# Kernel optimization log

Hardware: AMD Instinct MI355X
Metric: run time of the kernel (lower is better)

Reference implementation:

```python
import jax, jax.numpy as jnp
import numpy as np

N = 100000          # nodes
E = 1600000         # edges (before self loops)
IN, H, C, OUT = 128, 4, 32, 40
EPS = 1e-5          # BatchNorm eps
NEG_SLOPE = 0.2     # GATConv leaky_relu slope
BN_SCALE = 1.0 / np.sqrt(1.0 + EPS)  # eval BN with running mean 0, var 1


def gat_conv(x, W, att_src, att_dst, bias, src, dst, concat=True):
    """PyG GATConv (add_self_loops already applied to src/dst)."""
    heads, out_ch = att_src.shape
    n = x.shape[0]
    h = (x @ W).reshape(n, heads, out_ch)                 # [N,H,C]
    a_src = jnp.einsum('nhc,hc->nh', h, att_src)          # [N,H]
    a_dst = jnp.einsum('nhc,hc->nh', h, att_dst)          # [N,H]
    e = jax.nn.leaky_relu(a_src[src] + a_dst[dst], NEG_SLOPE)  # [E,H]
    # segment softmax over destination neighborhoods
    m = jax.ops.segment_max(e, dst, num_segments=n)
    e = jnp.exp(e - m[dst])
    s = jax.ops.segment_sum(e, dst, num_segments=n)
    alpha = e / (s[dst] + 1e-16)                          # [E,H]
    msg = h[src] * alpha[:, :, None]                      # [E,H,C]
    out = jax.ops.segment_sum(msg, dst, num_segments=n)   # [N,H,C]
    out = out.reshape(n, heads * out_ch) if concat else out.mean(axis=1)
    return out + bias


def setup_inputs():
    key = jax.random.key(0)
    ks = jax.random.split(key, 20)
    d = {}
    d['x'] = jax.random.normal(ks[0], (N, IN), dtype=jnp.float32)
    d['edge_index'] = jax.random.randint(ks[1], (2, E), 0, N, dtype=jnp.int32)
    sc = lambda fan: 1.0 / np.sqrt(fan)
    # layer 0: IN -> H*C
    d['W0'] = jax.random.normal(ks[2], (IN, H * C), dtype=jnp.float32) * sc(IN)
    d['as0'] = jax.random.normal(ks[3], (H, C), dtype=jnp.float32) * sc(C)
    d['ad0'] = jax.random.normal(ks[4], (H, C), dtype=jnp.float32) * sc(C)
    d['b0'] = jnp.zeros((H * C,), jnp.float32)
    d['g0'] = jnp.ones((H * C,), jnp.float32)
    d['be0'] = jnp.zeros((H * C,), jnp.float32)
    # layer 1: H*C -> H*C
    d['W1'] = jax.random.normal(ks[5], (H * C, H * C), dtype=jnp.float32) * sc(H * C)
    d['as1'] = jax.random.normal(ks[6], (H, C), dtype=jnp.float32) * sc(C)
    d['ad1'] = jax.random.normal(ks[7], (H, C), dtype=jnp.float32) * sc(C)
    d['b1'] = jnp.zeros((H * C,), jnp.float32)
    d['g1'] = jnp.ones((H * C,), jnp.float32)
    d['be1'] = jnp.zeros((H * C,), jnp.float32)
    # layer 2: H*C -> OUT, heads=1
    d['W2'] = jax.random.normal(ks[8], (H * C, OUT), dtype=jnp.float32) * sc(H * C)
    d['as2'] = jax.random.normal(ks[9], (1, OUT), dtype=jnp.float32) * sc(OUT)
    d['ad2'] = jax.random.normal(ks[10], (1, OUT), dtype=jnp.float32) * sc(OUT)
    d['b2'] = jnp.zeros((OUT,), jnp.float32)
    d['blast'] = jnp.zeros((OUT,), jnp.float32)
    return d


def reference(x, edge_index, W0, as0, ad0, b0, g0, be0,
              W1, as1, ad1, b1, g1, be1, W2, as2, ad2, b2, blast):
    loop = jnp.arange(N, dtype=edge_index.dtype)
    src = jnp.concatenate([edge_index[0], loop])
    dst = jnp.concatenate([edge_index[1], loop])
    h = gat_conv(x, W0, as0, ad0, b0, src, dst)
    h = jax.nn.relu(g0 * (h * BN_SCALE) + be0)   # eval BatchNorm + ReLU
    h = gat_conv(h, W1, as1, ad1, b1, src, dst)
    h = jax.nn.relu(g1 * (h * BN_SCALE) + be1)
    h = gat_conv(h, W2, as2, ad2, b2, src, dst)  # heads=1
    h = h + blast                                # ElementWiseLinear bias
    return jax.nn.log_softmax(h, axis=-1)
```

## Files before the change

### kernel.cpp

```cpp
#include <hip/hip_runtime.h>
#include <math.h>


static constexpr float BN_SCALE_F = 0.9999950000374996f;
static constexpr float NEG_SLOPE_F = 0.2f;

__global__ void k_deg(const int* __restrict__ ei, int E, int N, int* __restrict__ deg) {
    int i = blockIdx.x * 256 + threadIdx.x;
    int M = E + N;
    if (i >= M) return;
    int d = (i < E) ? ei[(size_t)E + i] : (i - E);
    atomicAdd(&deg[d], 1);
}

__global__ void k_scan1(const int* __restrict__ deg, int N, int* __restrict__ off,
                        int* __restrict__ bsum) {
    __shared__ int sh[2048];
    __shared__ int ts[256];
    int t = threadIdx.x;
    int base = blockIdx.x * 2048;
    for (int i = t; i < 2048; i += 256) sh[i] = (base + i < N) ? deg[base + i] : 0;
    __syncthreads();
    int loc[8];
    int tot = 0;
#pragma unroll
    for (int j = 0; j < 8; j++) { loc[j] = sh[t * 8 + j]; tot += loc[j]; }
    ts[t] = tot;
    __syncthreads();
    for (int d = 1; d < 256; d <<= 1) {
        int u = (t >= d) ? ts[t - d] : 0;
        __syncthreads();
        ts[t] += u;
        __syncthreads();
    }
    int run = (t > 0) ? ts[t - 1] : 0;
#pragma unroll
    for (int j = 0; j < 8; j++) {
        int idx = base + t * 8 + j;
        if (idx < N) off[idx] = run;
        run += loc[j];
    }
    if (t == 255) bsum[blockIdx.x] = ts[255];
}

__global__ void k_scan2(int* __restrict__ bsum, int nb) {
    __shared__ int ts[256];
    int t = threadIdx.x;
    int v = (t < nb) ? bsum[t] : 0;
    ts[t] = v;
    __syncthreads();
    for (int d = 1; d < 256; d <<= 1) {
        int u = (t >= d) ? ts[t - d] : 0;
        __syncthreads();
        ts[t] += u;
        __syncthreads();
    }
    if (t < nb) bsum[t] = ts[t] - v;
}

__global__ void k_scan3(int* __restrict__ off, const int* __restrict__ bsum, int N, int M) {
    int i = blockIdx.x * 256 + threadIdx.x;
    if (i < N) off[i] += bsum[i >> 11];
    else if (i == N) off[N] = M;
}

__global__ void k_scatter(const int* __restrict__ ei, int E, int N,
                          const int* __restrict__ off, int* __restrict__ cnt,
                          int* __restrict__ ssrc) {
    int i = blockIdx.x * 256 + threadIdx.x;
    int M = E + N;
    if (i >= M) return;
    int s, d;
    if (i < E) { s = ei[i]; d = ei[(size_t)E + i]; }
    else       { s = d = i - E; }
    int pos = off[d] + atomicAdd(&cnt[d], 1);
    ssrc[pos] = s;
}

template <int NC>
__global__ __launch_bounds__(512) void k_gemm(const float* __restrict__ A,
                                              const float* __restrict__ W, int N, int CC,
                                              int OST, float* __restrict__ out) {
    __shared__ float xs[128 * 128];
    __shared__ float ws[128 * NC];
    int tid = threadIdx.x;
    int row0 = blockIdx.x * 128;
    const float4* A4 = (const float4*)A;
#pragma unroll
    for (int i = 0; i < 8; i++) {
        int idx = tid + i * 512;
        int r = idx >> 5, c4 = idx & 31;
        int gr = row0 + r;
        float4 v = make_float4(0.f, 0.f, 0.f, 0.f);
        if (gr < N) v = A4[(size_t)gr * 32 + c4];
        int g = (r >> 3) & 3;
        *(float4*)&xs[r * 128 + ((c4 ^ g) << 2)] = v;
    }
    constexpr int WIT = (128 * NC) / (512 * 4);
#pragma unroll
    for (int i = 0; i < WIT; i++) {
        int idx = tid + i * 512;
        int k = idx / (NC / 4);
        int c = (idx % (NC / 4)) * 4;
        float4 v;
        if (c + 3 < CC) {
            v = *(const float4*)&W[(size_t)k * CC + c];
        } else {
            float tmp[4];
#pragma unroll
            for (int j = 0; j < 4; j++) tmp[j] = (c + j < CC) ? W[(size_t)k * CC + c + j] : 0.f;
            v = make_float4(tmp[0], tmp[1], tmp[2], tmp[3]);
        }
        *(float4*)&ws[k * NC + c] = v;
    }
    __syncthreads();

    int ty = tid >> 4;
    int tx = tid & 15;
    constexpr int NH = NC / 64;
    float4 acc[4][NH];
#pragma unroll
    for (int r = 0; r < 4; r++)
#pragma unroll
        for (int h = 0; h < NH; h++) acc[r][h] = make_float4(0.f, 0.f, 0.f, 0.f);

#pragma unroll 2
    for (int k4 = 0; k4 < 32; k4++) {
        float4 xv[4];
#pragma unroll
        for (int r = 0; r < 4; r++) {
            int row = ty * 4 + r;
            int g = (row >> 3) & 3;
            xv[r] = *(const float4*)&xs[row * 128 + (((k4 ^ g) & 31) << 2)];
        }
        float4 wv[4][NH];
#pragma unroll
        for (int j = 0; j < 4; j++)
#pragma unroll
            for (int h = 0; h < NH; h++)
                wv[j][h] = *(const float4*)&ws[(k4 * 4 + j) * NC + tx * 4 + 64 * h];
#pragma unroll
        for (int r = 0; r < 4; r++) {
            const float* xf = (const float*)&xv[r];
#pragma unroll
            for (int j = 0; j < 4; j++) {
                float xsv = xf[j];
#pragma unroll
                for (int h = 0; h < NH; h++) {
                    acc[r][h].x += xsv * wv[j][h].x;
                    acc[r][h].y += xsv * wv[j][h].y;
                    acc[r][h].z += xsv * wv[j][h].z;
                    acc[r][h].w += xsv * wv[j][h].w;
                }
            }
        }
    }
#pragma unroll
    for (int r = 0; r < 4; r++) {
        int gr = row0 + ty * 4 + r;
        if (gr >= N) continue;
#pragma unroll
        for (int h = 0; h < NH; h++) {
            int c = tx * 4 + 64 * h;
            if (c < CC) *(float4*)&out[(size_t)gr * OST + c] = acc[r][h];
        }
    }
}

__global__ void k_att(const float* __restrict__ h, const float* __restrict__ att_s,
                      const float* __restrict__ att_d, int N, float* __restrict__ asrc,
                      float* __restrict__ adst) {
    int wid = (blockIdx.x * 256 + threadIdx.x) >> 6;
    int lane = threadIdx.x & 63;
    if (wid >= N) return;
    float2 hv = *(const float2*)&h[(size_t)wid * 128 + lane * 2];
    float2 as_ = *(const float2*)&att_s[lane * 2];
    float2 ad_ = *(const float2*)&att_d[lane * 2];
    float ps = hv.x * as_.x + hv.y * as_.y;
    float pd = hv.x * ad_.x + hv.y * ad_.y;
    for (int d = 1; d < 16; d <<= 1) {
        ps += __shfl_xor(ps, d);
        pd += __shfl_xor(pd, d);
    }
    if ((lane & 15) == 0) {
        int hd = lane >> 4;
        asrc[(size_t)wid * 4 + hd] = ps;
        adst[(size_t)wid * 4 + hd] = pd;
    }
}

__global__ void k_att2(const float* __restrict__ h2, const float* __restrict__ as2,
                       const float* __restrict__ ad2, int N, float* __restrict__ asrc,
                       float* __restrict__ adst) {
    int wid = (blockIdx.x * 256 + threadIdx.x) >> 6;
    int lane = threadIdx.x & 63;
    if (wid >= N) return;
    float ps = 0.f, pd = 0.f;
    if (lane < 40) {
        float v = h2[(size_t)wid * 40 + lane];
        ps = v * as2[lane];
        pd = v * ad2[lane];
    }
    for (int d = 1; d < 64; d <<= 1) {
        ps += __shfl_xor(ps, d);
        pd += __shfl_xor(pd, d);
    }
    if (lane == 0) { asrc[wid] = ps; adst[wid] = pd; }
}

__global__ void k_agg(const float* __restrict__ h, const float* __restrict__ asrc,
                      const float* __restrict__ adst, const int* __restrict__ ssrc,
                      const int* __restrict__ off, const float* __restrict__ bias,
                      const float* __restrict__ gamma, const float* __restrict__ beta,
                      float* __restrict__ out, int N) {
    int wid = (blockIdx.x * 256 + threadIdx.x) >> 6;
    int lane = threadIdx.x & 63;
    if (wid >= N) return;
    int beg = off[wid], end = off[wid + 1];
    int hd = lane >> 4;
    float adst_h = adst[(size_t)wid * 4 + hd];
    float m = -INFINITY, ssum = 0.f, accx = 0.f, accy = 0.f;
    for (int j = beg; j < end; ++j) {
        int s = ssrc[j];
        float e = asrc[(size_t)s * 4 + hd] + adst_h;
        e = (e > 0.f) ? e : e * NEG_SLOPE_F;
        float mnew = fmaxf(m, e);
        float sc = __expf(m - mnew);
        float p = __expf(e - mnew);
        float2 hv = *(const float2*)&h[(size_t)s * 128 + lane * 2];
        ssum = ssum * sc + p;
        accx = accx * sc + p * hv.x;
        accy = accy * sc + p * hv.y;
        m = mnew;
    }
    float inv = 1.0f / (ssum + 1e-16f);
    int ch = lane * 2;
    float v0 = accx * inv + bias[ch];
    float v1 = accy * inv + bias[ch + 1];
    v0 = gamma[ch] * (v0 * BN_SCALE_F) + beta[ch];
    v1 = gamma[ch + 1] * (v1 * BN_SCALE_F) + beta[ch + 1];
    v0 = fmaxf(v0, 0.f);
    v1 = fmaxf(v1, 0.f);
    *(float2*)&out[(size_t)wid * 128 + ch] = make_float2(v0, v1);
}

__global__ void k_agg2(const float* __restrict__ h2, const float* __restrict__ asrc,
                       const float* __restrict__ adst, const int* __restrict__ ssrc,
                       const int* __restrict__ off, const float* __restrict__ b2,
                       const float* __restrict__ blast, float* __restrict__ out, int N) {
    int wid = (blockIdx.x * 256 + threadIdx.x) >> 6;
    int lane = threadIdx.x & 63;
    if (wid >= N) return;
    int beg = off[wid], end = off[wid + 1];
    float adn = adst[wid];
    int ch = lane;
    float m = -INFINITY, ssum = 0.f, acc = 0.f;
    for (int j = beg; j < end; ++j) {
        int s = ssrc[j];
        float e = asrc[s] + adn;
        e = (e > 0.f) ? e : e * NEG_SLOPE_F;
        float mnew = fmaxf(m, e);
        float sc = __expf(m - mnew);
        float p = __expf(e - mnew);
        float hv = (ch < 40) ? h2[(size_t)s * 40 + ch] : 0.f;
        ssum = ssum * sc + p;
        acc = acc * sc + p * hv;
        m = mnew;
    }
    float o = 0.f;
    if (ch < 40) o = acc / (ssum + 1e-16f) + b2[ch] + blast[ch];
    float lm = (ch < 40) ? o : -INFINITY;
    for (int d = 1; d < 64; d <<= 1) lm = fmaxf(lm, __shfl_xor(lm, d));
    float ex = (ch < 40) ? __expf(o - lm) : 0.f;
    float es = ex;
    for (int d = 1; d < 64; d <<= 1) es += __shfl_xor(es, d);
    if (ch < 40) out[(size_t)wid * 40 + ch] = o - lm - __logf(es);
}

extern "C" void kernel_launch(void* const* d_in, const int* in_sizes, int n_in, void* d_out,
                              int out_size, void* d_ws, size_t ws_size, hipStream_t stream) {
    const float* x   = (const float*)d_in[0];
    const int*   ei  = (const int*)d_in[1];
    const float* W0  = (const float*)d_in[2];
    const float* as0 = (const float*)d_in[3];
    const float* ad0 = (const float*)d_in[4];
    const float* b0  = (const float*)d_in[5];
    const float* g0  = (const float*)d_in[6];
    const float* be0 = (const float*)d_in[7];
    const float* W1  = (const float*)d_in[8];
    const float* as1 = (const float*)d_in[9];
    const float* ad1 = (const float*)d_in[10];
    const float* b1  = (const float*)d_in[11];
    const float* g1  = (const float*)d_in[12];
    const float* be1 = (const float*)d_in[13];
    const float* W2  = (const float*)d_in[14];
    const float* as2 = (const float*)d_in[15];
    const float* ad2 = (const float*)d_in[16];
    const float* b2  = (const float*)d_in[17];
    const float* bl  = (const float*)d_in[18];
    float* out = (float*)d_out;

    int N = in_sizes[0] / 128;
    int E = in_sizes[1] / 2;
    int M = E + N;

    char* p = (char*)d_ws;
    auto carve = [&](size_t bytes) -> char* {
        char* q = p;
        p += (bytes + 255) & ~(size_t)255;
        return q;
    };
    float* bufA = (float*)carve((size_t)N * 128 * 4);
    float* bufB = (float*)carve((size_t)N * 128 * 4);
    float* asrc = (float*)carve((size_t)N * 4 * 4);
    float* adst = (float*)carve((size_t)N * 4 * 4);
    int* deg  = (int*)carve((size_t)N * 4);
    int* off  = (int*)carve((size_t)(N + 1) * 4);
    int* bsum = (int*)carve(256 * 4);
    int* cnt  = (int*)carve((size_t)N * 4);
    int* ssrc = (int*)carve((size_t)M * 4);

    hipMemsetAsync(deg, 0, (size_t)N * 4, stream);
    hipMemsetAsync(cnt, 0, (size_t)N * 4, stream);
    k_deg<<<(M + 255) / 256, 256, 0, stream>>>(ei, E, N, deg);
    int NB = (N + 2047) / 2048;
    k_scan1<<<NB, 256, 0, stream>>>(deg, N, off, bsum);
    k_scan2<<<1, 256, 0, stream>>>(bsum, NB);
    k_scan3<<<(N + 256) / 256, 256, 0, stream>>>(off, bsum, N, M);
    k_scatter<<<(M + 255) / 256, 256, 0, stream>>>(ei, E, N, off, cnt, ssrc);

    int gblocks = (N + 127) / 128;
    int nodeblocks = (N + 3) / 4;

    k_gemm<128><<<gblocks, 512, 0, stream>>>(x, W0, N, 128, 128, bufA);
    k_att<<<nodeblocks, 256, 0, stream>>>(bufA, as0, ad0, N, asrc, adst);
    k_agg<<<nodeblocks, 256, 0, stream>>>(bufA, asrc, adst, ssrc, off, b0, g0, be0, bufB, N);
    k_gemm<128><<<gblocks, 512, 0, stream>>>(bufB, W1, N, 128, 128, bufA);
    k_att<<<nodeblocks, 256, 0, stream>>>(bufA, as1, ad1, N, asrc, adst);
    k_agg<<<nodeblocks, 256, 0, stream>>>(bufA, asrc, adst, ssrc, off, b1, g1, be1, bufB, N);
    k_gemm<64><<<gblocks, 512, 0, stream>>>(bufB, W2, N, 40, 40, bufA);
    k_att2<<<nodeblocks, 256, 0, stream>>>(bufA, as2, ad2, N, asrc, adst);
    k_agg2<<<nodeblocks, 256, 0, stream>>>(bufA, asrc, adst, ssrc, off, b2, bl, out, N);
}
```

Before: 1.080 ms.

## Process edges in chunks of 16 with wave-parallel softmax in GAT aggregation

The aggregation kernels now load 16 edges' source indices and attention logits in parallel across the wavefront, compute a chunk-wise max and exp-sum with shuffle reductions, and then gather neighbour features for the 16 edges in an unrolled loop. This replaces the serial per-edge load, exp and rescale chain with batched independent loads, which exposes more memory-level parallelism and cuts the number of exp calls per edge. Two accumulators split the dependency chain. It adds shuffle overhead and wastes lanes when a node has few neighbours (average degree is about 17).

```diff
diff --git a/kernel.cpp b/kernel.cpp
--- a/kernel.cpp
+++ b/kernel.cpp
@@ -217,26 +217,71 @@
     int lane = threadIdx.x & 63;
     if (wid >= N) return;
     int beg = off[wid], end = off[wid + 1];
+    int hd4 = lane & 3;
+    int ei = lane >> 2;
     int hd = lane >> 4;
-    float adst_h = adst[(size_t)wid * 4 + hd];
-    float m = -INFINITY, ssum = 0.f, accx = 0.f, accy = 0.f;
-    for (int j = beg; j < end; ++j) {
-        int s = ssrc[j];
-        float e = asrc[(size_t)s * 4 + hd] + adst_h;
-        e = (e > 0.f) ? e : e * NEG_SLOPE_F;
-        float mnew = fmaxf(m, e);
+    float adst_h4 = adst[(size_t)wid * 4 + hd4];
+    float m = -INFINITY, ssum = 0.f;
+    float accx0 = 0.f, accy0 = 0.f, accx1 = 0.f, accy1 = 0.f;
+    const float* hrow = h + lane * 2;
+    for (int c0 = beg; c0 < end; c0 += 16) {
+        int j = c0 + ei;
+        bool valid = j < end;
+        int s = 0;
+        float e = -INFINITY;
+        if (valid) {
+            s = ssrc[j];
+            e = asrc[(size_t)s * 4 + hd4] + adst_h4;
+            e = (e > 0.f) ? e : e * NEG_SLOPE_F;
+        }
+        float cmax = e;
+        cmax = fmaxf(cmax, __shfl_xor(cmax, 4));
+        cmax = fmaxf(cmax, __shfl_xor(cmax, 8));
+        cmax = fmaxf(cmax, __shfl_xor(cmax, 16));
+        cmax = fmaxf(cmax, __shfl_xor(cmax, 32));
+        float mnew = fmaxf(m, cmax);
         float sc = __expf(m - mnew);
         float p = __expf(e - mnew);
-        float2 hv = *(const float2*)&h[(size_t)s * 128 + lane * 2];
-        ssum = ssum * sc + p;
-        accx = accx * sc + p * hv.x;
-        accy = accy * sc + p * hv.y;
+        float psum = p;
+        psum += __shfl_xor(psum, 4);
+        psum += __shfl_xor(psum, 8);
+        psum += __shfl_xor(psum, 16);
+        psum += __shfl_xor(psum, 32);
+        ssum = ssum * sc + psum;
         m = mnew;
-    }
-    float inv = 1.0f / (ssum + 1e-16f);
+        float sc_my = __shfl(sc, hd);
+        accx0 *= sc_my; accy0 *= sc_my;
+        accx1 *= sc_my; accy1 *= sc_my;
+        if (end - c0 >= 16) {
+#pragma unroll
+            for (int t = 0; t < 16; t++) {
+                int sl = 4 * t + hd;
+                int sj = __shfl(s, sl);
+                float pj = __shfl(p, sl);
+                float2 hv = *(const float2*)&hrow[(size_t)sj * 128];
+                if (t & 1) { accx1 += pj * hv.x; accy1 += pj * hv.y; }
+                else       { accx0 += pj * hv.x; accy0 += pj * hv.y; }
+            }
+        } else {
+            int nv = end - c0;
+#pragma unroll
+            for (int t = 0; t < 16; t++) {
+                if (t < nv) {
+                    int sl = 4 * t + hd;
+                    int sj = __shfl(s, sl);
+                    float pj = __shfl(p, sl);
+                    float2 hv = *(const float2*)&hrow[(size_t)sj * 128];
+                    if (t & 1) { accx1 += pj * hv.x; accy1 += pj * hv.y; }
+                    else       { accx0 += pj * hv.x; accy0 += pj * hv.y; }
+                }
+            }
+        }
+    }
+    float s_h = __shfl(ssum, hd);
+    float inv = 1.0f / (s_h + 1e-16f);
     int ch = lane * 2;
-    float v0 = accx * inv + bias[ch];
-    float v1 = accy * inv + bias[ch + 1];
+    float v0 = (accx0 + accx1) * inv + bias[ch];
+    float v1 = (accy0 + accy1) * inv + bias[ch + 1];
     v0 = gamma[ch] * (v0 * BN_SCALE_F) + beta[ch];
     v1 = gamma[ch + 1] * (v1 * BN_SCALE_F) + beta[ch + 1];
     v0 = fmaxf(v0, 0.f);
@@ -253,22 +298,62 @@
     if (wid >= N) return;
     int beg = off[wid], end = off[wid + 1];
     float adn = adst[wid];
+    int ei = lane & 15;
     int ch = lane;
-    float m = -INFINITY, ssum = 0.f, acc = 0.f;
-    for (int j = beg; j < end; ++j) {
-        int s = ssrc[j];
-        float e = asrc[s] + adn;
-        e = (e > 0.f) ? e : e * NEG_SLOPE_F;
-        float mnew = fmaxf(m, e);
+    float m = -INFINITY, ssum = 0.f, acc0 = 0.f, acc1 = 0.f;
+    for (int c0 = beg; c0 < end; c0 += 16) {
+        int j = c0 + ei;
+        bool valid = j < end;
+        int s = 0;
+        float e = -INFINITY;
+        if (valid) {
+            s = ssrc[j];
+            e = asrc[s] + adn;
+            e = (e > 0.f) ? e : e * NEG_SLOPE_F;
+        }
+        float cmax = e;
+        cmax = fmaxf(cmax, __shfl_xor(cmax, 1));
+        cmax = fmaxf(cmax, __shfl_xor(cmax, 2));
+        cmax = fmaxf(cmax, __shfl_xor(cmax, 4));
+        cmax = fmaxf(cmax, __shfl_xor(cmax, 8));
+        float mnew = fmaxf(m, cmax);
         float sc = __expf(m - mnew);
         float p = __expf(e - mnew);
-        float hv = (ch < 40) ? h2[(size_t)s * 40 + ch] : 0.f;
-        ssum = ssum * sc + p;
-        acc = acc * sc + p * hv;
+        float psum = p;
+        psum += __shfl_xor(psum, 1);
+        psum += __shfl_xor(psum, 2);
+        psum += __shfl_xor(psum, 4);
+        psum += __shfl_xor(psum, 8);
+        ssum = ssum * sc + psum;
         m = mnew;
+        acc0 *= sc; acc1 *= sc;
+        if (end - c0 >= 16) {
+#pragma unroll
+            for (int t = 0; t < 16; t++) {
+                int sj = __shfl(s, t);
+                float pj = __shfl(p, t);
+                float hv = 0.f;
+                if (ch < 40) hv = h2[(size_t)sj * 40 + ch];
+                if (t & 1) acc1 += pj * hv;
+                else       acc0 += pj * hv;
+            }
+        } else {
+            int nv = end - c0;
+#pragma unroll
+            for (int t = 0; t < 16; t++) {
+                if (t < nv) {
+                    int sj = __shfl(s, t);
+                    float pj = __shfl(p, t);
+                    float hv = 0.f;
+                    if (ch < 40) hv = h2[(size_t)sj * 40 + ch];
+                    if (t & 1) acc1 += pj * hv;
+                    else       acc0 += pj * hv;
+                }
+            }
+        }
     }
     float o = 0.f;
-    if (ch < 40) o = acc / (ssum + 1e-16f) + b2[ch] + blast[ch];
+    if (ch < 40) o = (acc0 + acc1) / (ssum + 1e-16f) + b2[ch] + blast[ch];
     float lm = (ch < 40) ? o : -INFINITY;
     for (int d = 1; d < 64; d <<= 1) lm = fmaxf(lm, __shfl_xor(lm, d));
     float ex = (ch < 40) ? __expf(o - lm) : 0.f;
```

Result: faster. 942.8 us (-12.7%).
